# Kernel optimization log

Measured on AMD Instinct MI355X. Metric: run time of the kernel, lower is better.

## Reference

```python
import jax, jax.numpy as jnp
import numpy as np

S = 128          # voxel grid resolution per axis
NPB = 50000      # active voxels per batch element
B = 2            # batch size
C_IN = 64
C_OUT = 64
K = 3            # kernel size

# kernel offsets in [-1,0,1]^3, shape [27, 3]
_OFFS = np.stack(np.meshgrid(np.arange(-1, 2), np.arange(-1, 2), np.arange(-1, 2), indexing='ij'), axis=-1).reshape(-1, 3)


def setup_inputs() -> dict:
    rng = np.random.default_rng(0)
    coords_list = []
    for b in range(B):
        lin = rng.choice(S * S * S, size=NPB, replace=False)  # unique voxels
        x = lin // (S * S)
        y = (lin // S) % S
        z = lin % S
        coords_list.append(np.stack([np.full(NPB, b), x, y, z], axis=1))
    coords = jnp.asarray(np.concatenate(coords_list, axis=0), dtype=jnp.int32)  # [N,4]

    key = jax.random.key(0)
    k1, k2, k3 = jax.random.split(key, 3)
    feats = jax.random.normal(k1, (B * NPB, C_IN), dtype=jnp.float32)
    fan1 = C_IN * K ** 3
    fan2 = C_OUT * K ** 3
    W1 = jax.random.normal(k2, (K ** 3, C_IN, C_OUT), dtype=jnp.float32) / np.sqrt(fan1)
    W2 = jax.random.normal(k3, (K ** 3, C_OUT, C_OUT), dtype=jnp.float32) / np.sqrt(fan2)
    return {"feats": feats, "coords": coords, "W1": W1, "W2": W2}


def _encode(coords):
    # linear key: ((b*S + x)*S + y)*S + z ; fits in int32 for S=128, B small
    b, x, y, z = coords[:, 0], coords[:, 1], coords[:, 2], coords[:, 3]
    return ((b * S + x) * S + y) * S + z


def _sparse_conv(feats, coords, W):
    """Stride-1 sparse (submanifold-style) 3D conv: output coords == input coords.
    feats [N,Cin], coords [N,4], W [27,Cin,Cout] -> [N,Cout]."""
    N = feats.shape[0]
    keys = _encode(coords)
    order = jnp.argsort(keys)
    skeys = keys[order]
    offs = jnp.asarray(_OFFS, dtype=jnp.int32)  # [27,3]

    def gather_one(d):
        qxyz = coords[:, 1:4] + d[None, :]
        valid = jnp.all((qxyz >= 0) & (qxyz < S), axis=1)
        qkey = keys + (d[0] * S * S + d[1] * S + d[2])
        idx = jnp.clip(jnp.searchsorted(skeys, qkey), 0, N - 1)
        found = valid & (skeys[idx] == qkey)
        return jnp.where(found[:, None], feats[order[idx]], 0.0)  # [N,Cin]

    gathered = jax.vmap(gather_one)(offs)  # [27, N, Cin]
    return jnp.einsum('onc,ocd->nd', gathered, W)


def reference(feats, coords, W1, W2):
    h = _sparse_conv(feats, coords, W1)
    out = _sparse_conv(h, coords, W2)
    return out
```

## Files before the change

### kernel.cpp

```cpp
#include <hip/hip_runtime.h>
#include <stdint.h>

#define SGRID 128
#define CAP 4096

typedef _Float16 f16;
typedef f16 f16x8 __attribute__((ext_vector_type(8)));
typedef float f32x4 __attribute__((ext_vector_type(4)));
typedef unsigned long long u64;
typedef unsigned short u16;

static __device__ __forceinline__ f32x4 mfma16(uint4 a, uint4 b, f32x4 c) {
    union { uint4 u; f16x8 v; } ua, ub;
    ua.u = a; ub.u = b;
    return __builtin_amdgcn_mfma_f32_16x16x32_f16(ua.v, ub.v, c, 0, 0, 0);
}

static __device__ __forceinline__ void split8(const float* v, uint4& hu, uint4& lu) {
    union { f16 h[8]; uint4 u; } hv, lv;
    #pragma unroll
    for (int j = 0; j < 8; ++j) {
        f16 h = (f16)v[j];
        hv.h[j] = h;
        lv.h[j] = (f16)(v[j] - (float)h);
    }
    hu = hv.u; lu = lv.u;
}

static __device__ __forceinline__ void gload16(const void* g, void* l) {
    __builtin_amdgcn_global_load_lds(
        (const __attribute__((address_space(1))) unsigned int*)g,
        (__attribute__((address_space(3))) unsigned int*)l, 16, 0, 0);
}

static __device__ __forceinline__ void read_row_frags(
    const float* __restrict__ sW, int rl, int lq, uint4 ah[2], uint4 al[2])
{
    #pragma unroll
    for (int ks = 0; ks < 2; ++ks) {
        int c0 = ks * 8 + lq * 2;
        int s0 = (c0 - rl) & 15, s1 = (c0 + 1 - rl) & 15;
        float4 v0 = *(const float4*)&sW[(rl * 16 + s0) * 4];
        float4 v1 = *(const float4*)&sW[(rl * 16 + s1) * 4];
        float v[8] = {v0.x, v0.y, v0.z, v0.w, v1.x, v1.y, v1.z, v1.w};
        split8(v, ah[ks], al[ks]);
    }
}

__global__ void k_clear(uint4* __restrict__ bitmap4, int nwords4,
                        int* __restrict__ cnt, float* __restrict__ zrow) {
    const int stride = gridDim.x * 256;
    for (int i = blockIdx.x * 256 + threadIdx.x; i < nwords4; i += stride)
        bitmap4[i] = (uint4){0, 0, 0, 0};
    if (blockIdx.x == 0 && threadIdx.x < 26) cnt[threadIdx.x * 16] = 0;
    if (blockIdx.x == 0 && threadIdx.x < 64) zrow[threadIdx.x] = 0.f;
}

__global__ void __launch_bounds__(256) k_scatprep(
    const int* __restrict__ coords, int* __restrict__ table,
    unsigned* __restrict__ bitmap, int N, int scatB,
    const float* __restrict__ W1, const float* __restrict__ W2,
    f16* __restrict__ Wp1, f16* __restrict__ Wp2)
{
    const int tid = threadIdx.x;
    if (blockIdx.x < scatB) {
        int i = blockIdx.x * 256 + tid;
        if (i < N) {
            int4 c = ((const int4*)coords)[i];
            int key = ((c.x * SGRID + c.y) * SGRID + c.z) * SGRID + c.w;
            table[key] = i;
            atomicOr(&bitmap[key >> 5], 1u << (key & 31));
        }
        return;
    }
    int idx = (blockIdx.x - scatB) * 256 + tid;
    const int half = 27 * 512;
    const float* W = (idx < half) ? W1 : W2;
    f16* Wp = (idx < half) ? Wp1 : Wp2;
    int id = (idx < half) ? idx : idx - half;
    int lane = id & 63;
    int ks = (id >> 6) & 1;
    int ct = (id >> 7) & 3;
    int o  = id >> 9;
    int co  = ct * 16 + (lane & 15);
    int ci0 = ks * 32 + (lane >> 4) * 8;
    union { f16 h[8]; uint4 u; } hv;
    #pragma unroll
    for (int j = 0; j < 8; ++j)
        hv.h[j] = (f16)W[((size_t)o * 64 + ci0 + j) * 64 + co];
    ((uint4*)Wp)[id] = hv.u;
}

__global__ void __launch_bounds__(256) k_build(
    const int* __restrict__ coords, const int* __restrict__ table,
    const unsigned* __restrict__ bitmap,
    int* __restrict__ pin, u16* __restrict__ ppos, unsigned* __restrict__ omaskA,
    int* __restrict__ cnt, int N)
{
    __shared__ u64 sbal[26][4];
    __shared__ int sbase4[26][4];

    const int tid = threadIdx.x, lane = tid & 63, wave = tid >> 6;
    const int n = blockIdx.x * 256 + tid;
    const bool valid = n < N;

    int4 c = {0, 0, 0, 0};
    if (valid) c = ((const int4*)coords)[n];
    const int z  = c.w;
    const int zb = (z == 0) ? 0 : z - 1;
    const int wofs = zb >> 5, sh = zb & 31;

    unsigned omask = 0;
    #pragma unroll
    for (int cidx = 0; cidx < 9; ++cidx) {
        int dx = cidx / 3 - 1, dy = cidx % 3 - 1;
        int qx = c.y + dx, qy = c.z + dy;
        bool colok = valid && ((unsigned)qx < SGRID) && ((unsigned)qy < SGRID);
        int wi = colok ? ((((c.x * SGRID + qx) * SGRID + qy) << 2) + wofs) : 0;
        unsigned w0 = bitmap[wi];
        unsigned w1 = bitmap[wi + 1];
        u64 w = (u64)w0 | ((u64)w1 << 32);
        unsigned t = (unsigned)(w >> sh) & 7u;
        if (z == 0)         t = (t << 1) & 6u;
        if (z == SGRID - 1) t &= 3u;
        t = colok ? t : 0u;
        omask |= t << (cidx * 3);
    }
    omask &= ~(1u << 13);

    const int key = ((c.x * SGRID + c.y) * SGRID + c.z) * SGRID + z;
    int nb[26];
    #pragma unroll
    for (int s = 0; s < 26; ++s) {
        int o = s < 13 ? s : s + 1;
        bool occ = (omask >> o) & 1u;
        int qkey = key + (o / 9 - 1) * SGRID * SGRID + ((o / 3) % 3 - 1) * SGRID + (o % 3 - 1);
        int v = table[occ ? qkey : 0];
        nb[s] = occ ? v : -1;
    }

    #pragma unroll
    for (int s = 0; s < 26; ++s) {
        u64 bal = __ballot(nb[s] >= 0);
        if (lane == 0) sbal[s][wave] = bal;
    }
    __syncthreads();

    if (tid < 26) {
        int c0 = (int)__popcll(sbal[tid][0]);
        int c1 = (int)__popcll(sbal[tid][1]);
        int c2 = (int)__popcll(sbal[tid][2]);
        int c3 = (int)__popcll(sbal[tid][3]);
        int tot = c0 + c1 + c2 + c3;
        int base = tot ? atomicAdd(&cnt[tid * 16], tot) : 0;
        sbase4[tid][0] = base;
        sbase4[tid][1] = base + c0;
        sbase4[tid][2] = base + c0 + c1;
        sbase4[tid][3] = base + c0 + c1 + c2;
    }
    __syncthreads();

    const u64 ltmask = (1ull << lane) - 1ull;
    unsigned fm = 0;
    #pragma unroll
    for (int s = 0; s < 26; ++s) {
        if (nb[s] >= 0) {
            int pos = sbase4[s][wave] + (int)__popcll(sbal[s][wave] & ltmask);
            if (pos < CAP) {
                pin[s * CAP + pos] = nb[s];
                ppos[(size_t)s * N + n] = (u16)pos;
                fm |= 1u << s;
            }
        }
    }
    if (valid) omaskA[n] = fm;
}

__global__ void __launch_bounds__(256) k_spart(
    const float* __restrict__ A, const f16* __restrict__ Wp,
    const int* __restrict__ pin, const int* __restrict__ cnt,
    float* __restrict__ P, const float* __restrict__ zrow)
{
    __shared__ float sF[4096];
    int w = (blockIdx.x * 256 + threadIdx.x) >> 6;
    if (w >= 26 * 256) return;
    const int lane = threadIdx.x & 63;
    const int wv = threadIdx.x >> 6;
    int slot  = w >> 8;
    int chunk = w & 255;
    int cn = cnt[slot * 16]; if (cn > CAP) cn = CAP;
    int i0 = chunk * 16;
    if (i0 >= cn) return;
    int o = slot < 13 ? slot : slot + 1;
    const int r = lane & 15, lq = lane >> 4;
    float* sW = sF + wv * 1024;

    #pragma unroll
    for (int i = 0; i < 4; ++i) {
        int rl = i * 4 + (lane >> 4);
        int slotc = lane & 15;
        int csrc = (slotc + rl) & 15;
        int p = i0 + rl;
        const float* src;
        if (p < cn) {
            int rid = pin[slot * CAP + p];
            src = A + (size_t)rid * 64 + csrc * 4;
        } else {
            src = zrow + csrc * 4;
        }
        gload16(src, sW + i * 256);
    }

    const uint4* wb = (const uint4*)Wp + (size_t)o * 512 + lane;
    uint4 b[2][4];
    #pragma unroll
    for (int ct = 0; ct < 4; ++ct)
        #pragma unroll
        for (int ks = 0; ks < 2; ++ks)
            b[ks][ct] = wb[(ct * 2 + ks) * 64];

    asm volatile("s_waitcnt vmcnt(0)" ::: "memory");
    __builtin_amdgcn_sched_barrier(0);

    uint4 ah[2], al[2];
    read_row_frags(sW, r, lq, ah, al);

    f32x4 acc[4];
    #pragma unroll
    for (int ct = 0; ct < 4; ++ct) acc[ct] = (f32x4){0.f, 0.f, 0.f, 0.f};
    #pragma unroll
    for (int ks = 0; ks < 2; ++ks)
        #pragma unroll
        for (int ct = 0; ct < 4; ++ct) {
            acc[ct] = mfma16(ah[ks], b[ks][ct], acc[ct]);
            acc[ct] = mfma16(al[ks], b[ks][ct], acc[ct]);
        }

    #pragma unroll
    for (int j = 0; j < 4; ++j) {
        int pr = i0 + lq * 4 + j;
        float* dst = P + ((size_t)(slot * CAP + pr) << 6);
        #pragma unroll
        for (int ct = 0; ct < 4; ++ct)
            dst[ct * 16 + r] = acc[ct][j];
    }
}

__global__ void __launch_bounds__(256) k_cgather(
    const float* __restrict__ A, const f16* __restrict__ Wp,
    const unsigned* __restrict__ omaskA, const u16* __restrict__ ppos,
    const float* __restrict__ P, float* __restrict__ O, int N)
{
    __shared__ float sF[8192];
    const int tid = threadIdx.x;
    const int wv = tid >> 6, lane = tid & 63;
    const int r = lane & 15, lq = lane >> 4;
    const int gw = blockIdx.x * 4 + wv;
    const int p0 = gw * 32;
    float* sW = sF + wv * 2048;

    #pragma unroll
    for (int j = 0; j < 8; ++j) {
        int ch = j * 64 + lane;
        int rl = ch >> 4, slot = ch & 15;
        int csrc = (slot + rl) & 15;
        int grow = p0 + rl;
        if (grow > N - 1) grow = N - 1;
        gload16(A + (size_t)grow * 64 + csrc * 4, sW + j * 256);
    }

    const uint4* wb = (const uint4*)Wp + 13 * 512 + lane;
    uint4 b[2][4];
    #pragma unroll
    for (int ct = 0; ct < 4; ++ct)
        #pragma unroll
        for (int ks = 0; ks < 2; ++ks)
            b[ks][ct] = wb[(ct * 2 + ks) * 64];

    asm volatile("s_waitcnt vmcnt(0)" ::: "memory");
    __builtin_amdgcn_sched_barrier(0);
    if (p0 >= N) return;

    uint4 ah[2][2], al[2][2];
    #pragma unroll
    for (int rt = 0; rt < 2; ++rt)
        read_row_frags(sW, rt * 16 + r, lq, ah[rt], al[rt]);

    f32x4 acc[2][4];
    #pragma unroll
    for (int i = 0; i < 2; ++i)
        #pragma unroll
        for (int j = 0; j < 4; ++j) acc[i][j] = (f32x4){0.f, 0.f, 0.f, 0.f};

    #pragma unroll
    for (int ks = 0; ks < 2; ++ks)
        #pragma unroll
        for (int rt = 0; rt < 2; ++rt)
            #pragma unroll
            for (int ct = 0; ct < 4; ++ct) {
                acc[rt][ct] = mfma16(ah[rt][ks], b[ks][ct], acc[rt][ct]);
                acc[rt][ct] = mfma16(al[rt][ks], b[ks][ct], acc[rt][ct]);
            }

    #pragma unroll
    for (int rt = 0; rt < 2; ++rt)
        #pragma unroll
        for (int j = 0; j < 4; ++j) {
            int row = p0 + rt * 16 + lq * 4 + j;
            if (row < N) {
                unsigned om = omaskA[row];
                while (om) {
                    int s = __ffs(om) - 1; om &= om - 1;
                    int pos = ppos[(size_t)s * N + row];
                    const float* pr_ = P + ((size_t)(s * CAP + pos) << 6);
                    #pragma unroll
                    for (int ct = 0; ct < 4; ++ct)
                        acc[rt][ct][j] += pr_[ct * 16 + r];
                }
            }
        }

    #pragma unroll
    for (int rt = 0; rt < 2; ++rt)
        #pragma unroll
        for (int j = 0; j < 4; ++j) {
            int row = p0 + rt * 16 + lq * 4 + j;
            if (row < N) {
                #pragma unroll
                for (int ct = 0; ct < 4; ++ct)
                    O[(size_t)row * 64 + ct * 16 + r] = acc[rt][ct][j];
            }
        }
}

extern "C" void kernel_launch(void* const* d_in, const int* in_sizes, int n_in,
                              void* d_out, int out_size, void* d_ws, size_t ws_size,
                              hipStream_t stream) {
    const float* feats  = (const float*)d_in[0];
    const int*   coords = (const int*)d_in[1];
    const float* W1     = (const float*)d_in[2];
    const float* W2     = (const float*)d_in[3];
    float* out = (float*)d_out;

    const int N = in_sizes[0] / 64;
    const size_t nvox = 2ull * SGRID * SGRID * SGRID;

    char* p = (char*)d_ws;
    int*      table  = (int*)p;      p += nvox * 4;
    unsigned* bitmap = (unsigned*)p; p += (nvox / 32) * 4;
    p += 16;
    int*      cnt    = (int*)p;      p += 26 * 16 * 4;
    float*    zrow   = (float*)p;    p += 64 * 4;
    int*      pin    = (int*)p;      p += 26ull * CAP * 4;
    u16*      ppos   = (u16*)p;      p += ((26ull * N * 2 + 15) & ~15ull);
    unsigned* omaskA = (unsigned*)p; p += (size_t)N * 4;
    float*    partial= (float*)p;    p += 26ull * CAP * 64 * 4;
    float*    H      = (float*)p;    p += (size_t)N * 64 * 4;
    f16*      Wp1    = (f16*)p;      p += 27ull * 4096 * 2;
    f16*      Wp2    = (f16*)p;      p += 27ull * 4096 * 2;

    const int bm4     = (int)(nvox / 32 / 4) + 1;
    const int scatB   = (N + 255) / 256;
    const int ngroups = (N + 31) / 32;
    const int centerB = (ngroups + 3) / 4;
    const int spartB  = 26 * 256 / 4;

    k_clear<<<256, 256, 0, stream>>>((uint4*)bitmap, bm4, cnt, zrow);
    k_scatprep<<<scatB + 108, 256, 0, stream>>>(coords, table, bitmap, N, scatB,
                                                W1, W2, Wp1, Wp2);
    k_build<<<scatB, 256, 0, stream>>>(coords, table, bitmap, pin, ppos, omaskA, cnt, N);
    k_spart<<<spartB, 256, 0, stream>>>(feats, Wp1, pin, cnt, partial, zrow);
    k_cgather<<<centerB, 256, 0, stream>>>(feats, Wp1, omaskA, ppos, partial, H, N);
    k_spart<<<spartB, 256, 0, stream>>>(H, Wp2, pin, cnt, partial, zrow);
    k_cgather<<<centerB, 256, 0, stream>>>(H, Wp2, omaskA, ppos, partial, out, N);
}
```

Measured before the change: 99.68 us.

## Reorder voxels by spatial column via counting sort for gather locality

Adds a histogram, scan and scatter pass that sorts voxels by their (b,x,y) column key and permutes the features into sorted order. The build, partial and gather kernels then run on sorted rows, so neighbour lookups and partial-sum reads hit nearby memory. The final output is scattered back through the permutation. This adds three launches, including a single-block serial scan, plus a full copy of the features, in exchange for better cache locality in the gather phases.

```diff
diff --git a/kernel.cpp b/kernel.cpp
--- a/kernel.cpp
+++ b/kernel.cpp
@@ -47,33 +47,28 @@
     }
 }
 
-__global__ void k_clear(uint4* __restrict__ bitmap4, int nwords4,
-                        int* __restrict__ cnt, float* __restrict__ zrow) {
+__global__ void k_clear(uint4* __restrict__ dst4, int nwords4) {
     const int stride = gridDim.x * 256;
     for (int i = blockIdx.x * 256 + threadIdx.x; i < nwords4; i += stride)
-        bitmap4[i] = (uint4){0, 0, 0, 0};
-    if (blockIdx.x == 0 && threadIdx.x < 26) cnt[threadIdx.x * 16] = 0;
-    if (blockIdx.x == 0 && threadIdx.x < 64) zrow[threadIdx.x] = 0.f;
-}
-
-__global__ void __launch_bounds__(256) k_scatprep(
-    const int* __restrict__ coords, int* __restrict__ table,
-    unsigned* __restrict__ bitmap, int N, int scatB,
+        dst4[i] = (uint4){0, 0, 0, 0};
+}
+
+__global__ void __launch_bounds__(256) k_histprep(
+    const int* __restrict__ coords, int* __restrict__ hist, int N, int histB,
     const float* __restrict__ W1, const float* __restrict__ W2,
     f16* __restrict__ Wp1, f16* __restrict__ Wp2)
 {
     const int tid = threadIdx.x;
-    if (blockIdx.x < scatB) {
+    if (blockIdx.x < histB) {
         int i = blockIdx.x * 256 + tid;
         if (i < N) {
             int4 c = ((const int4*)coords)[i];
             int key = ((c.x * SGRID + c.y) * SGRID + c.z) * SGRID + c.w;
-            table[key] = i;
-            atomicOr(&bitmap[key >> 5], 1u << (key & 31));
+            atomicAdd(&hist[key >> 7], 1);
         }
         return;
     }
-    int idx = (blockIdx.x - scatB) * 256 + tid;
+    int idx = (blockIdx.x - histB) * 256 + tid;
     const int half = 27 * 512;
     const float* W = (idx < half) ? W1 : W2;
     f16* Wp = (idx < half) ? Wp1 : Wp2;
@@ -91,8 +86,59 @@
     ((uint4*)Wp)[id] = hv.u;
 }
 
+__global__ void __launch_bounds__(256) k_scan(const int* __restrict__ hist,
+                                              int* __restrict__ base)
+{
+    __shared__ int wsum[4];
+    const int t = threadIdx.x, lane = t & 63, wv = t >> 6;
+    const int off = t * 128;
+    int sum = 0;
+    for (int i = 0; i < 128; ++i) sum += hist[off + i];
+    int inc = sum;
+    #pragma unroll
+    for (int d = 1; d < 64; d <<= 1) {
+        int v = __shfl_up(inc, d, 64);
+        if (lane >= d) inc += v;
+    }
+    if (lane == 63) wsum[wv] = inc;
+    __syncthreads();
+    int wpre = 0;
+    #pragma unroll
+    for (int wwi = 0; wwi < 4; ++wwi)
+        if (wwi < wv) wpre += wsum[wwi];
+    int run = wpre + inc - sum;
+    for (int i = 0; i < 128; ++i) {
+        int v = hist[off + i];
+        base[off + i] = run;
+        run += v;
+    }
+}
+
+__global__ void __launch_bounds__(256) k_scatter(
+    const int* __restrict__ coords, const float* __restrict__ F,
+    const int* __restrict__ base, int* __restrict__ rcnt,
+    int* __restrict__ perm, int* __restrict__ skey,
+    int* __restrict__ table, unsigned* __restrict__ bitmap,
+    float* __restrict__ Fs, int N)
+{
+    int n = blockIdx.x * 256 + threadIdx.x;
+    if (n >= N) return;
+    int4 c = ((const int4*)coords)[n];
+    int key = ((c.x * SGRID + c.y) * SGRID + c.z) * SGRID + c.w;
+    int col = key >> 7;
+    int pos = base[col] + atomicAdd(&rcnt[col], 1);
+    perm[pos] = n;
+    skey[pos] = key;
+    table[key] = pos;
+    atomicOr(&bitmap[key >> 5], 1u << (key & 31));
+    const uint4* src = (const uint4*)(F + (size_t)n * 64);
+    uint4* dst = (uint4*)(Fs + (size_t)pos * 64);
+    #pragma unroll
+    for (int i = 0; i < 16; ++i) dst[i] = src[i];
+}
+
 __global__ void __launch_bounds__(256) k_build(
-    const int* __restrict__ coords, const int* __restrict__ table,
+    const int* __restrict__ skey, const int* __restrict__ table,
     const unsigned* __restrict__ bitmap,
     int* __restrict__ pin, u16* __restrict__ ppos, unsigned* __restrict__ omaskA,
     int* __restrict__ cnt, int N)
@@ -104,9 +150,11 @@
     const int n = blockIdx.x * 256 + tid;
     const bool valid = n < N;
 
-    int4 c = {0, 0, 0, 0};
-    if (valid) c = ((const int4*)coords)[n];
-    const int z  = c.w;
+    int key = valid ? skey[n] : 0;
+    const int z = key & 127;
+    const int y = (key >> 7) & 127;
+    const int x = (key >> 14) & 127;
+    const int col = key >> 7;
     const int zb = (z == 0) ? 0 : z - 1;
     const int wofs = zb >> 5, sh = zb & 31;
 
@@ -114,9 +162,9 @@
     #pragma unroll
     for (int cidx = 0; cidx < 9; ++cidx) {
         int dx = cidx / 3 - 1, dy = cidx % 3 - 1;
-        int qx = c.y + dx, qy = c.z + dy;
+        int qx = x + dx, qy = y + dy;
         bool colok = valid && ((unsigned)qx < SGRID) && ((unsigned)qy < SGRID);
-        int wi = colok ? ((((c.x * SGRID + qx) * SGRID + qy) << 2) + wofs) : 0;
+        int wi = colok ? (((col + dx * SGRID + dy) << 2) + wofs) : 0;
         unsigned w0 = bitmap[wi];
         unsigned w1 = bitmap[wi + 1];
         u64 w = (u64)w0 | ((u64)w1 << 32);
@@ -128,7 +176,6 @@
     }
     omask &= ~(1u << 13);
 
-    const int key = ((c.x * SGRID + c.y) * SGRID + c.z) * SGRID + z;
     int nb[26];
     #pragma unroll
     for (int s = 0; s < 26; ++s) {
@@ -152,11 +199,11 @@
         int c2 = (int)__popcll(sbal[tid][2]);
         int c3 = (int)__popcll(sbal[tid][3]);
         int tot = c0 + c1 + c2 + c3;
-        int base = tot ? atomicAdd(&cnt[tid * 16], tot) : 0;
-        sbase4[tid][0] = base;
-        sbase4[tid][1] = base + c0;
-        sbase4[tid][2] = base + c0 + c1;
-        sbase4[tid][3] = base + c0 + c1 + c2;
+        int b0 = tot ? atomicAdd(&cnt[tid * 16], tot) : 0;
+        sbase4[tid][0] = b0;
+        sbase4[tid][1] = b0 + c0;
+        sbase4[tid][2] = b0 + c0 + c1;
+        sbase4[tid][3] = b0 + c0 + c1 + c2;
     }
     __syncthreads();
 
@@ -249,7 +296,8 @@
 __global__ void __launch_bounds__(256) k_cgather(
     const float* __restrict__ A, const f16* __restrict__ Wp,
     const unsigned* __restrict__ omaskA, const u16* __restrict__ ppos,
-    const float* __restrict__ P, float* __restrict__ O, int N)
+    const float* __restrict__ P, float* __restrict__ O,
+    const int* __restrict__ perm, int N)
 {
     __shared__ float sF[8192];
     const int tid = threadIdx.x;
@@ -326,9 +374,10 @@
         for (int j = 0; j < 4; ++j) {
             int row = p0 + rt * 16 + lq * 4 + j;
             if (row < N) {
+                size_t drow = perm ? (size_t)perm[row] : (size_t)row;
                 #pragma unroll
                 for (int ct = 0; ct < 4; ++ct)
-                    O[(size_t)row * 64 + ct * 16 + r] = acc[rt][ct][j];
+                    O[drow * 64 + ct * 16 + r] = acc[rt][ct][j];
             }
         }
 }
@@ -344,33 +393,46 @@
 
     const int N = in_sizes[0] / 64;
     const size_t nvox = 2ull * SGRID * SGRID * SGRID;
+    const int NCOL = 2 * SGRID * SGRID;
 
     char* p = (char*)d_ws;
     int*      table  = (int*)p;      p += nvox * 4;
+    char*     clr0   = p;
     unsigned* bitmap = (unsigned*)p; p += (nvox / 32) * 4;
     p += 16;
     int*      cnt    = (int*)p;      p += 26 * 16 * 4;
     float*    zrow   = (float*)p;    p += 64 * 4;
-    int*      pin    = (int*)p;      p += 26ull * CAP * 4;
+    int*      hist   = (int*)p;      p += (size_t)NCOL * 4;
+    int*      rcnt   = (int*)p;      p += (size_t)NCOL * 4;
+    char*     clr1   = p;
+    int*      base   = (int*)p;      p += (size_t)NCOL * 4;
+    int*      perm   = (int*)p;      p += (size_t)N * 4;
+    int*      skey   = (int*)p;      p += (size_t)N * 4;
     u16*      ppos   = (u16*)p;      p += ((26ull * N * 2 + 15) & ~15ull);
     unsigned* omaskA = (unsigned*)p; p += (size_t)N * 4;
+    int*      pin    = (int*)p;      p += 26ull * CAP * 4;
     float*    partial= (float*)p;    p += 26ull * CAP * 64 * 4;
-    float*    H      = (float*)p;    p += (size_t)N * 64 * 4;
+    float*    Fs     = (float*)p;    p += (size_t)N * 64 * 4;
+    float*    Hs     = (float*)p;    p += (size_t)N * 64 * 4;
     f16*      Wp1    = (f16*)p;      p += 27ull * 4096 * 2;
     f16*      Wp2    = (f16*)p;      p += 27ull * 4096 * 2;
 
-    const int bm4     = (int)(nvox / 32 / 4) + 1;
-    const int scatB   = (N + 255) / 256;
+    const int clrWords4 = (int)((clr1 - clr0) / 16);
+    const int ptB     = (N + 255) / 256;
     const int ngroups = (N + 31) / 32;
     const int centerB = (ngroups + 3) / 4;
     const int spartB  = 26 * 256 / 4;
 
-    k_clear<<<256, 256, 0, stream>>>((uint4*)bitmap, bm4, cnt, zrow);
-    k_scatprep<<<scatB + 108, 256, 0, stream>>>(coords, table, bitmap, N, scatB,
-                                                W1, W2, Wp1, Wp2);
-    k_build<<<scatB, 256, 0, stream>>>(coords, table, bitmap, pin, ppos, omaskA, cnt, N);
-    k_spart<<<spartB, 256, 0, stream>>>(feats, Wp1, pin, cnt, partial, zrow);
-    k_cgather<<<centerB, 256, 0, stream>>>(feats, Wp1, omaskA, ppos, partial, H, N);
-    k_spart<<<spartB, 256, 0, stream>>>(H, Wp2, pin, cnt, partial, zrow);
-    k_cgather<<<centerB, 256, 0, stream>>>(H, Wp2, omaskA, ppos, partial, out, N);
-}
+    k_clear<<<256, 256, 0, stream>>>((uint4*)clr0, clrWords4);
+    k_histprep<<<ptB + 108, 256, 0, stream>>>(coords, hist, N, ptB, W1, W2, Wp1, Wp2);
+    k_scan<<<1, 256, 0, stream>>>(hist, base);
+    k_scatter<<<ptB, 256, 0, stream>>>(coords, feats, base, rcnt, perm, skey,
+                                       table, bitmap, Fs, N);
+    k_build<<<ptB, 256, 0, stream>>>(skey, table, bitmap, pin, ppos, omaskA, cnt, N);
+    k_spart<<<spartB, 256, 0, stream>>>(Fs, Wp1, pin, cnt, partial, zrow);
+    k_cgather<<<centerB, 256, 0, stream>>>(Fs, Wp1, omaskA, ppos, partial, Hs,
+                                           nullptr, N);
+    k_spart<<<spartB, 256, 0, stream>>>(Hs, Wp2, pin, cnt, partial, zrow);
+    k_cgather<<<centerB, 256, 0, stream>>>(Hs, Wp2, omaskA, ppos, partial, out,
+                                           perm, N);
+}
```

After: 140.0 us. +40.4%, slower.
